# Performance work log

Hardware: AMD Instinct MI355X
Metric: run time of the kernel (lower is better)

Reference implementation:

```python
import jax, jax.numpy as jnp
import numpy as np

C, T, D = 32, 768, 100      # n_countries, n_times, n_ages (=n_features)
H = 5                        # attention heads (EncoderLayer default)
HID_GCN = 60                 # GCN hidden features
FFN = 64                     # feed_forward_dim
NPRED = 10                   # n_predictions
LHID = 200                   # hid_linear_part_dim
NL = 3                       # encoder layers


def setup_inputs() -> dict:
    key = jax.random.key(0)
    ks = jax.random.split(key, 24)
    s = 0.05
    rn = lambda k, shp: jax.random.normal(k, shp, jnp.float32) * s
    return {
        "X": jax.random.normal(ks[0], (C, T, D), jnp.float32),
        "A": jax.random.uniform(ks[1], (C, C), jnp.float32),
        # GCN params
        "gcn_w1": rn(ks[2], (D, HID_GCN)),
        "gcn_b1": rn(ks[3], (HID_GCN,)),
        "gcn_w2": rn(ks[4], (HID_GCN, D)),
        "gcn_b2": rn(ks[5], (D,)),
        # 3 stacked encoder layers
        "enc_wq": rn(ks[6], (NL, H, D, D)),
        "enc_wk": rn(ks[7], (NL, H, D, D)),
        "enc_wv": rn(ks[8], (NL, H, D, D)),
        "enc_wm": rn(ks[9], (NL, H * D, D)),
        "enc_f1w": rn(ks[10], (NL, D, FFN)),
        "enc_f1b": rn(ks[11], (NL, FFN)),
        "enc_f2w": rn(ks[12], (NL, FFN, D)),
        "enc_f2b": rn(ks[13], (NL, D)),
        "enc_ln1g": jnp.ones((NL, D), jnp.float32),
        "enc_ln1b": jnp.zeros((NL, D), jnp.float32),
        "enc_ln2g": jnp.ones((NL, D), jnp.float32),
        "enc_ln2b": jnp.zeros((NL, D), jnp.float32),
        "lin1_w": rn(ks[14], (D, LHID)),
        "lin1_b": rn(ks[15], (LHID,)),
        "lin2_w": rn(ks[16], (LHID, D)),
        "lin2_b": rn(ks[17], (D,)),
    }


def _layer_norm(x, g, b, eps=1e-5):
    m = x.mean(-1, keepdims=True)
    v = ((x - m) ** 2).mean(-1, keepdims=True)
    return (x - m) / jnp.sqrt(v + eps) * g + b


def _encoder_layer(x, wq, wk, wv, wm, f1w, f1b, f2w, f2b, g1, b1, g2, b2):
    # x: [C, T, D]; wq/wk/wv: [H, D, D]
    Q = jnp.einsum('ctd,hde->chte', x, wq)
    K = jnp.einsum('ctd,hde->chte', x, wk)
    V = jnp.einsum('ctd,hde->chte', x, wv)
    scores = jnp.einsum('chte,chse->chts', Q, K) / jnp.sqrt(jnp.float32(D))
    attn = jax.nn.softmax(scores, axis=-1)
    out = jnp.einsum('chts,chse->chte', attn, V)        # [C,H,T,D]
    out = out.transpose(0, 2, 1, 3).reshape(x.shape[0], x.shape[1], H * D)
    x = _layer_norm(x + out @ wm, g1, b1)
    ffn = jax.nn.relu(x @ f1w + f1b) @ f2w + f2b
    return _layer_norm(x + ffn, g2, b2)


def reference(X, A, gcn_w1, gcn_b1, gcn_w2, gcn_b2,
              enc_wq, enc_wk, enc_wv, enc_wm,
              enc_f1w, enc_f1b, enc_f2w, enc_f2b,
              enc_ln1g, enc_ln1b, enc_ln2g, enc_ln2b,
              lin1_w, lin1_b, lin2_w, lin2_b):
    n = A.shape[0]
    adj = A + jnp.eye(n, dtype=A.dtype)
    adj_hat = adj / adj.sum(-1, keepdims=True)
    # GCN layer 1
    h = jnp.einsum('ij,jta->ita', adj_hat, X)
    h = jnp.einsum('ita,ao->ito', h, gcn_w1) + gcn_b1
    h = jax.nn.relu(h)
    # GCN layer 2
    h = jnp.einsum('ij,jta->ita', adj_hat, h)
    h = jnp.einsum('ita,ao->ito', h, gcn_w2) + gcn_b2
    # 3 encoder layers (fixed structural loop)
    for l in range(NL):
        h = _encoder_layer(h, enc_wq[l], enc_wk[l], enc_wv[l], enc_wm[l],
                           enc_f1w[l], enc_f1b[l], enc_f2w[l], enc_f2b[l],
                           enc_ln1g[l], enc_ln1b[l], enc_ln2g[l], enc_ln2b[l])
    last = h[:, -1, :]  # [C, D]
    def step(carry, _):
        p = (carry @ lin1_w + lin1_b) @ lin2_w + lin2_b
        return p, p
    _, preds = jax.lax.scan(step, last, None, length=NPRED)  # [NPRED, C, D]
    return preds.transpose(1, 0, 2)  # [C, NPRED, D]
```

## Files before the change

kernel.cpp:

```cpp
#include <hip/hip_runtime.h>


#define ROWS 24576

#define OFF_ADJ   0L
#define OFF_X0    1024L
#define OFF_X1    (OFF_X0 + 2457600L)
#define OFF_XROW  (OFF_X1 + 3932160L)
#define OFF_XT    (OFF_XROW + 1572864L)
#define OFF_WBF   (OFF_XT + 1572864L)
#define OFF_MHT   (OFF_WBF + 6291456L)
#define OFF_USTT  (OFF_MHT + 122880L)
#define OFF_MP    (OFF_USTT + 98304L)
#define OFF_C0    (OFF_MP + 10000L)
#define OFF_F1WT  (OFF_C0 + 128L)
#define OFF_F2WT  (OFF_F1WT + 12288L)
#define OFF_GW1T  (OFF_F2WT + 10752L)
#define OFF_GW2T  (OFF_GW1T + 4096L)

typedef __attribute__((ext_vector_type(8))) short short8;
typedef __attribute__((ext_vector_type(4))) short short4v;
typedef __attribute__((ext_vector_type(4))) float float4v;
typedef __attribute__((ext_vector_type(2))) unsigned int uint2v;
typedef __attribute__((ext_vector_type(4))) unsigned int uint4v;

__device__ inline unsigned short f2bf(float f) {
    unsigned u = __builtin_bit_cast(unsigned, f);
    return (unsigned short)((u + 0x7fffu + ((u >> 16) & 1u)) >> 16);
}
__device__ inline unsigned pk2bf(float lo, float hi) {
    unsigned r;
    asm("v_cvt_pk_bf16_f32 %0, %1, %2" : "=v"(r) : "v"(lo), "v"(hi));
    return r;
}
__device__ inline void st4s(short* p, unsigned a, unsigned b) {
    *(short4v*)p = __builtin_bit_cast(short4v, (uint2v){a, b});
}
__device__ inline float bf2f(unsigned short v) {
    return __builtin_bit_cast(float, ((unsigned)v) << 16);
}
__device__ inline void gload16(const short* g, short* l) {
    __builtin_amdgcn_global_load_lds((const __attribute__((address_space(1))) void*)g,
                                     (__attribute__((address_space(3))) void*)l, 16, 0, 0);
}

__global__ void __launch_bounds__(256) k_mu2(const float* __restrict__ wq, const float* __restrict__ wk,
                                             const float* __restrict__ wv, const float* __restrict__ wm,
                                             const float* __restrict__ l1w, const float* __restrict__ l1b,
                                             const float* __restrict__ l2w, const float* __restrict__ l2b,
                                             const float* __restrict__ f1w, const float* __restrict__ f2w,
                                             const float* __restrict__ A,
                                             const float* __restrict__ gw1, const float* __restrict__ gw2,
                                             unsigned short* __restrict__ MhT, unsigned short* __restrict__ UstT,
                                             float* __restrict__ Mp, float* __restrict__ c0v,
                                             unsigned short* __restrict__ f1wT, unsigned short* __restrict__ f2wT,
                                             float* __restrict__ adjh,
                                             unsigned short* __restrict__ gw1T, unsigned short* __restrict__ gw2T) {
    int bi = blockIdx.x, tid = threadIdx.x;
    if (bi < 480) {
        int mat = bi >> 4, sub = bi & 15;
        int mode = mat / 15, idx = mat % 15, l = idx / 5, h = idx % 5;
        const float* Asrc = (mode == 0 ? wq : wv) + (l*5 + h)*10000;
        const float* Bsrc = (mode == 0) ? (wk + (l*5 + h)*10000) : (wm + l*50000 + h*10000);
        int oend = sub*625 + 625;
        for (int o = sub*625 + tid; o < oend; o += 256) {
            int r = o / 100, cix = o - (o/100)*100;
            const float* arow = Asrc + r*100;
            float acc = 0.f;
            if (mode == 0) {
                const float* brow = Bsrc + cix*100;
                for (int e = 0; e < 100; ++e) acc += arow[e] * brow[e];
                MhT[(long)(l*5 + h)*16384 + cix*128 + r] = f2bf(acc * 0.1f);
            } else {
                for (int e = 0; e < 100; ++e) acc += arow[e] * Bsrc[e*100 + cix];
                UstT[(long)l*65536 + (long)cix*512 + h*100 + r] = f2bf(acc);
            }
        }
        if (sub == 0) {
            if (mode == 0) {
                unsigned short* M0 = MhT + (long)(l*5 + h)*16384;
                for (int i = tid; i < 28*128; i += 256) M0[(100 + i/128)*128 + (i%128)] = 0;
                for (int i = tid; i < 100*28; i += 256) M0[(i/28)*128 + 100 + (i%28)] = 0;
            } else if (h == 4) {
                unsigned short* U0 = UstT + (long)l*65536;
                for (int i = tid; i < 28*512; i += 256) U0[(long)(100 + i/512)*512 + (i%512)] = 0;
                for (int i = tid; i < 100*12; i += 256) U0[(long)(i/12)*512 + 500 + (i%12)] = 0;
            }
        }
    } else if (bi < 496) {
        int sub = bi - 480;
        int oend = sub*625 + 625;
        for (int o = sub*625 + tid; o < oend; o += 256) {
            int r = o / 100, cix = o - (o/100)*100;
            const float* arow = l1w + r*200;
            float acc = 0.f;
            for (int e = 0; e < 200; ++e) acc += arow[e] * l2w[e*100 + cix];
            Mp[r*100 + cix] = acc;
        }
    } else if (bi == 496) {
        if (tid < 100) {
            float acc = l2b[tid];
            for (int e = 0; e < 200; ++e) acc += l1b[e] * l2w[e*100 + tid];
            c0v[tid] = acc;
        }
    } else if (bi < 500) {
        int l = bi - 497;
        unsigned short* F1 = f1wT + (long)l*8192;
        for (int i = tid; i < 8192; i += 256) {
            int o = i >> 7, k = i & 127;
            F1[i] = (k < 100) ? f2bf(f1w[l*6400 + k*64 + o]) : (unsigned short)0;
        }
        unsigned short* F2 = f2wT + (long)l*7168;
        for (int i = tid; i < 7168; i += 256) {
            int o2 = i >> 6, k2 = i & 63;
            F2[i] = (o2 < 100) ? f2bf(f2w[l*6400 + k2*100 + o2]) : (unsigned short)0;
        }
    } else if (bi == 500) {
        __shared__ float adj[1024];
        __shared__ float rs[32];
        for (int i = tid; i < 1024; i += 256) {
            int r = i >> 5, j = i & 31;
            adj[i] = A[i] + (r == j ? 1.f : 0.f);
        }
        __syncthreads();
        if (tid < 32) {
            float s = 0.f;
            #pragma unroll
            for (int jj = 0; jj < 32; ++jj) s += adj[tid*32 + jj];
            rs[tid] = s;
        }
        __syncthreads();
        for (int i = tid; i < 1024; i += 256) adjh[i] = adj[i] / rs[i >> 5];
    } else {
        for (int i = tid; i < 8192; i += 256) {
            int o = i >> 7, k = i & 127;
            gw1T[i] = (o < 60 && k < 100) ? f2bf(gw1[k*60 + o]) : (unsigned short)0;
        }
        for (int i = tid; i < 7168; i += 256) {
            int o = i >> 6, k = i & 63;
            gw2T[i] = (o < 100 && k < 60) ? f2bf(gw2[k*100 + o]) : (unsigned short)0;
        }
    }
}

__global__ void __launch_bounds__(128) k_gw1(const float* __restrict__ X,
                                             const unsigned short* __restrict__ gw1T,
                                             unsigned short* __restrict__ g) {
    const int tid = threadIdx.x, wave = tid >> 6, lane = tid & 63;
    const int l15 = lane & 15, l4 = lane >> 4;
    const long row = (long)blockIdx.x*32 + wave*16 + l15;
    const float* xrp = X + row*100;
    float4v acc[4];
    #pragma unroll
    for (int mt = 0; mt < 4; ++mt) acc[mt] = (float4v){0,0,0,0};
    #pragma unroll
    for (int ks = 0; ks < 4; ++ks) {
        short8 b;
        #pragma unroll
        for (int e = 0; e < 8; ++e) {
            int k = ks*32 + l4*8 + e;
            b[e] = (k < 100) ? (short)f2bf(xrp[k]) : (short)0;
        }
        #pragma unroll
        for (int mt = 0; mt < 4; ++mt) {
            short8 a = *(const short8*)((const short*)gw1T + (mt*16 + l15)*128 + ks*32 + l4*8);
            acc[mt] = __builtin_amdgcn_mfma_f32_16x16x32_bf16(a, b, acc[mt], 0, 0, 0);
        }
    }
    #pragma unroll
    for (int mt = 0; mt < 4; ++mt) {
        int o0 = mt*16 + l4*4;
        *(uint2v*)(g + row*64 + o0) =
            (uint2v){pk2bf(acc[mt][0], acc[mt][1]), pk2bf(acc[mt][2], acc[mt][3])};
    }
}

__global__ void __launch_bounds__(256) k_spmmg(const float* __restrict__ adjh,
                                               const unsigned short* __restrict__ g,
                                               const float* __restrict__ b1,
                                               unsigned short* __restrict__ hid) {
    __shared__ float adj[1024];
    int tid = threadIdx.x;
    for (int i = tid; i < 1024; i += 256) adj[i] = adjh[i];
    __syncthreads();
    long p = (long)blockIdx.x*256 + tid;
    int o = (int)(p & 63);
    float acc[32];
    #pragma unroll
    for (int i = 0; i < 32; ++i) acc[i] = 0.f;
    for (int j = 0; j < 32; ++j) {
        float xv = bf2f(g[(long)j*49152 + p]);
        #pragma unroll
        for (int i = 0; i < 32; ++i) acc[i] += adj[i*32 + j] * xv;
    }
    float bias = (o < 60) ? b1[o] : 0.f;
    #pragma unroll
    for (int i = 0; i < 32; ++i) hid[(long)i*49152 + p] = f2bf(fmaxf(acc[i] + bias, 0.f));
}

__global__ void __launch_bounds__(128) k_gw2(const unsigned short* __restrict__ hid,
                                             const unsigned short* __restrict__ gw2T,
                                             unsigned short* __restrict__ h2) {
    const int tid = threadIdx.x, wave = tid >> 6, lane = tid & 63;
    const int l15 = lane & 15, l4 = lane >> 4;
    const long row = (long)blockIdx.x*32 + wave*16 + l15;
    float4v acc[7];
    #pragma unroll
    for (int mt = 0; mt < 7; ++mt) acc[mt] = (float4v){0,0,0,0};
    #pragma unroll
    for (int ks = 0; ks < 2; ++ks) {
        short8 b = *(const short8*)((const short*)hid + row*64 + ks*32 + l4*8);
        #pragma unroll
        for (int mt = 0; mt < 7; ++mt) {
            short8 a = *(const short8*)((const short*)gw2T + (mt*16 + l15)*64 + ks*32 + l4*8);
            acc[mt] = __builtin_amdgcn_mfma_f32_16x16x32_bf16(a, b, acc[mt], 0, 0, 0);
        }
    }
    #pragma unroll
    for (int mt = 0; mt < 7; ++mt) {
        int o0 = mt*16 + l4*4;
        *(uint2v*)(h2 + row*128 + o0) =
            (uint2v){pk2bf(acc[mt][0], acc[mt][1]), pk2bf(acc[mt][2], acc[mt][3])};
    }
    *(uint2v*)(h2 + row*128 + 112 + l4*4) = (uint2v){0u, 0u};
}

__global__ void __launch_bounds__(384) k_spmmx(const float* __restrict__ adjh,
                                               const unsigned short* __restrict__ h2,
                                               const float* __restrict__ b2,
                                               float* __restrict__ x0,
                                               unsigned short* __restrict__ xrow,
                                               unsigned short* __restrict__ xT) {
    __shared__ float adj[1024];
    int tid = threadIdx.x;
    for (int i = tid; i < 1024; i += 384) adj[i] = adjh[i];
    __syncthreads();
    long p = (long)blockIdx.x*384 + tid;
    int o = (int)(p & 127);
    int t = (int)(p >> 7);
    float acc[32];
    #pragma unroll
    for (int i = 0; i < 32; ++i) acc[i] = 0.f;
    for (int j = 0; j < 32; ++j) {
        float xv = bf2f(h2[(long)j*98304 + p]);
        #pragma unroll
        for (int i = 0; i < 32; ++i) acc[i] += adj[i*32 + j] * xv;
    }
    if (o < 100) {
        float bias = b2[o];
        #pragma unroll
        for (int i = 0; i < 32; ++i) {
            float v = acc[i] + bias;
            x0[((long)i*768 + t)*100 + o] = v;
            unsigned short bv = f2bf(v);
            xrow[((long)i*768 + t)*128 + o] = bv;
            xT[(long)i*98304 + (long)o*768 + t] = bv;
        }
    } else {
        #pragma unroll
        for (int i = 0; i < 32; ++i) {
            xrow[((long)i*768 + t)*128 + o] = 0;
            if (o < 112) xT[(long)i*98304 + (long)o*768 + t] = 0;
        }
    }
}


__global__ void __launch_bounds__(256) k_attn12(const unsigned short* __restrict__ xrow,
                                                const unsigned short* __restrict__ xT,
                                                const unsigned short* __restrict__ MhT,
                                                unsigned short* __restrict__ Wb) {
    __shared__ __align__(16) short xr[2][64 * 128];
    __shared__ __align__(16) short xt[112 * 64];
    const int tid = threadIdx.x;
    const int wave = tid >> 6, lane = tid & 63;
    const int l15 = lane & 15, l4 = lane >> 4;
    const int c = blockIdx.z, h = blockIdx.y, q0 = blockIdx.x * 128;

    const short* xrg = (const short*)xrow + (long)c*768*128;
    const short* xtg = (const short*)xT + (long)c*128*768;
    const int rl4 = lane >> 4, cp16 = lane & 15;
    const int rl8 = lane >> 3, cp8 = lane & 7;
    const int njt = (wave == 3) ? 2 : 4;
    const int sw8 = (l15 & 7) << 3;
    const int swt = l15 & 7;

    #pragma unroll
    for (int j = 0; j < 4; ++j) {
        int row = wave*16 + j*4 + rl4;
        int lc = cp16 ^ (row & 7);
        gload16(xrg + (long)row*128 + lc*8, xr[0] + (wave*16 + j*4)*128);
    }

    short8 qb0[4], qb1[4];
    {
        short* mq = &xr[1][wave * 16 * 128];
        const short* Mb = (const short*)MhT + (long)h*16384 + l15*128 + l4*8;
        const short* xq = (const short*)xrow + ((long)c*768 + q0 + wave*16 + l15)*128 + l4*8;
        short8 bq0[4], bq1[4];
        #pragma unroll
        for (int kk = 0; kk < 4; ++kk) {
            bq0[kk] = *(const short8*)(xq + kk*32);
            bq1[kk] = *(const short8*)(xq + 64*128 + kk*32);
        }
        float4v qc0[8], qc1[8];
        #pragma unroll
        for (int mt = 0; mt < 8; ++mt) { qc0[mt] = (float4v){0,0,0,0}; qc1[mt] = (float4v){0,0,0,0}; }
        #pragma unroll
        for (int mt = 0; mt < 8; ++mt) {
            #pragma unroll
            for (int kk = 0; kk < 4; ++kk) {
                short8 a = *(const short8*)(Mb + (mt*16)*128 + kk*32);
                qc0[mt] = __builtin_amdgcn_mfma_f32_16x16x32_bf16(a, bq0[kk], qc0[mt], 0, 0, 0);
                qc1[mt] = __builtin_amdgcn_mfma_f32_16x16x32_bf16(a, bq1[kk], qc1[mt], 0, 0, 0);
            }
        }
        #pragma unroll
        for (int mt = 0; mt < 8; ++mt)
            st4s(mq + l15*128 + ((mt*16 + l4*4) ^ sw8),
                 pk2bf(qc0[mt][0], qc0[mt][1]), pk2bf(qc0[mt][2], qc0[mt][3]));
        asm volatile("" ::: "memory");
        #pragma unroll
        for (int kk = 0; kk < 4; ++kk)
            qb0[kk] = *(const short8*)(mq + l15*128 + ((kk*32 + l4*8) ^ sw8));
        asm volatile("" ::: "memory");
        #pragma unroll
        for (int mt = 0; mt < 8; ++mt)
            st4s(mq + l15*128 + ((mt*16 + l4*4) ^ sw8),
                 pk2bf(qc1[mt][0], qc1[mt][1]), pk2bf(qc1[mt][2], qc1[mt][3]));
        asm volatile("" ::: "memory");
        #pragma unroll
        for (int kk = 0; kk < 4; ++kk)
            qb1[kk] = *(const short8*)(mq + l15*128 + ((kk*32 + l4*8) ^ sw8));
    }

    __syncthreads();

    float4v o0[7], o1[7];
    #pragma unroll
    for (int n = 0; n < 7; ++n) { o0[n] = (float4v){0,0,0,0}; o1[n] = (float4v){0,0,0,0}; }
    float lsum0 = 0.f, lsum1 = 0.f;

    for (int kt = 0; kt < 12; ++kt) {
        const int key0 = kt * 64;
        const short* xrb = xr[kt & 1];

        for (int j = 0; j < njt; ++j) {
            int row = wave*32 + j*8 + rl8;
            int lc = cp8 ^ (row & 7);
            gload16(xtg + (long)row*768 + key0 + lc*8, xt + (wave*32 + j*8)*64);
        }
        if (kt < 11) {
            short* xrn = xr[(kt + 1) & 1];
            #pragma unroll
            for (int j = 0; j < 4; ++j) {
                int row = wave*16 + j*4 + rl4;
                int lc = cp16 ^ (row & 7);
                gload16(xrg + (long)(key0 + 64 + row)*128 + lc*8, xrn + (wave*16 + j*4)*128);
            }
        }
        __builtin_amdgcn_sched_barrier(0);

        unsigned pw0[4], pw1[4];
        #pragma unroll
        for (int kn = 0; kn < 2; ++kn) {
            float4v s0 = (float4v){0,0,0,0}, s1 = (float4v){0,0,0,0};
            #pragma unroll
            for (int kk = 0; kk < 4; ++kk) {
                short8 a = *(const short8*)(xrb + (kn*16 + l15)*128 + (((kk*4 + l4) ^ (l15 & 7))*8));
                s0 = __builtin_amdgcn_mfma_f32_16x16x32_bf16(a, qb0[kk], s0, 0, 0, 0);
                s1 = __builtin_amdgcn_mfma_f32_16x16x32_bf16(a, qb1[kk], s1, 0, 0, 0);
            }
            float p0[4], p1[4];
            #pragma unroll
            for (int r = 0; r < 4; ++r) {
                p0[r] = __expf(s0[r]); lsum0 += p0[r];
                p1[r] = __expf(s1[r]); lsum1 += p1[r];
            }
            pw0[kn*2]   = pk2bf(p0[0], p0[1]); pw0[kn*2+1] = pk2bf(p0[2], p0[3]);
            pw1[kn*2]   = pk2bf(p1[0], p1[1]); pw1[kn*2+1] = pk2bf(p1[2], p1[3]);
        }

        if (kt < 11) { asm volatile("s_waitcnt vmcnt(4)" ::: "memory"); }
        else         { asm volatile("s_waitcnt vmcnt(0)" ::: "memory"); }
        __builtin_amdgcn_s_barrier();

        {
            short8 b0 = __builtin_bit_cast(short8, (uint4v){pw0[0], pw0[1], pw0[2], pw0[3]});
            short8 b1 = __builtin_bit_cast(short8, (uint4v){pw1[0], pw1[1], pw1[2], pw1[3]});
            const int offLo = (((l4 >> 1) ^ swt) * 8) + (l4 & 1) * 4;
            const int offHi = (((2 + (l4 >> 1)) ^ swt) * 8) + (l4 & 1) * 4;
            #pragma unroll
            for (int dt = 0; dt < 7; ++dt) {
                const short* xrow_t = xt + (dt*16 + l15)*64;
                short4v lo = *(const short4v*)(xrow_t + offLo);
                short4v hi = *(const short4v*)(xrow_t + offHi);
                short8 a = __builtin_shufflevector(lo, hi, 0, 1, 2, 3, 4, 5, 6, 7);
                o0[dt] = __builtin_amdgcn_mfma_f32_16x16x32_bf16(a, b0, o0[dt], 0, 0, 0);
                o1[dt] = __builtin_amdgcn_mfma_f32_16x16x32_bf16(a, b1, o1[dt], 0, 0, 0);
            }
        }

        #pragma unroll
        for (int kn = 2; kn < 4; ++kn) {
            float4v s0 = (float4v){0,0,0,0}, s1 = (float4v){0,0,0,0};
            #pragma unroll
            for (int kk = 0; kk < 4; ++kk) {
                short8 a = *(const short8*)(xrb + (kn*16 + l15)*128 + (((kk*4 + l4) ^ (l15 & 7))*8));
                s0 = __builtin_amdgcn_mfma_f32_16x16x32_bf16(a, qb0[kk], s0, 0, 0, 0);
                s1 = __builtin_amdgcn_mfma_f32_16x16x32_bf16(a, qb1[kk], s1, 0, 0, 0);
            }
            float p0[4], p1[4];
            #pragma unroll
            for (int r = 0; r < 4; ++r) {
                p0[r] = __expf(s0[r]); lsum0 += p0[r];
                p1[r] = __expf(s1[r]); lsum1 += p1[r];
            }
            pw0[(kn-2)*2]   = pk2bf(p0[0], p0[1]); pw0[(kn-2)*2+1] = pk2bf(p0[2], p0[3]);
            pw1[(kn-2)*2]   = pk2bf(p1[0], p1[1]); pw1[(kn-2)*2+1] = pk2bf(p1[2], p1[3]);
        }

        {
            short8 b0 = __builtin_bit_cast(short8, (uint4v){pw0[0], pw0[1], pw0[2], pw0[3]});
            short8 b1 = __builtin_bit_cast(short8, (uint4v){pw1[0], pw1[1], pw1[2], pw1[3]});
            const int offLo = (((4 + (l4 >> 1)) ^ swt) * 8) + (l4 & 1) * 4;
            const int offHi = (((6 + (l4 >> 1)) ^ swt) * 8) + (l4 & 1) * 4;
            #pragma unroll
            for (int dt = 0; dt < 7; ++dt) {
                const short* xrow_t = xt + (dt*16 + l15)*64;
                short4v lo = *(const short4v*)(xrow_t + offLo);
                short4v hi = *(const short4v*)(xrow_t + offHi);
                short8 a = __builtin_shufflevector(lo, hi, 0, 1, 2, 3, 4, 5, 6, 7);
                o0[dt] = __builtin_amdgcn_mfma_f32_16x16x32_bf16(a, b0, o0[dt], 0, 0, 0);
                o1[dt] = __builtin_amdgcn_mfma_f32_16x16x32_bf16(a, b1, o1[dt], 0, 0, 0);
            }
        }
        __syncthreads();
    }

    float l0 = lsum0, l1 = lsum1;
    l0 += __shfl_xor(l0, 16, 64); l0 += __shfl_xor(l0, 32, 64);
    l1 += __shfl_xor(l1, 16, 64); l1 += __shfl_xor(l1, 32, 64);
    float inv0 = 1.f / l0, inv1 = 1.f / l1;

    unsigned short* Wo0 = Wb + ((long)(c*768 + q0 + wave*16 + l15))*512 + h*100 + l4*4;
    unsigned short* Wo1 = Wo0 + 64*512;
    #pragma unroll
    for (int dt = 0; dt < 7; ++dt) {
        if (dt < 6 || l4 == 0) {
            *(uint2v*)(Wo0 + dt*16) = (uint2v){pk2bf(o0[dt][0]*inv0, o0[dt][1]*inv0),
                                               pk2bf(o0[dt][2]*inv0, o0[dt][3]*inv0)};
            *(uint2v*)(Wo1 + dt*16) = (uint2v){pk2bf(o1[dt][0]*inv1, o1[dt][1]*inv1),
                                               pk2bf(o1[dt][2]*inv1, o1[dt][3]*inv1)};
        }
    }
    if (h == 0) {
        unsigned short* Wz = Wb + ((long)c*768 + q0)*512 + 500;
        for (int i = tid; i < 1536; i += 256) Wz[(long)(i/12)*512 + (i%12)] = 0;
    }
}

template<bool EMIT>
__global__ void __launch_bounds__(128) k_tail(const unsigned short* __restrict__ Wb,
        const unsigned short* __restrict__ UstT,
        const unsigned short* __restrict__ f1wT, const unsigned short* __restrict__ f2wT,
        const float* __restrict__ f1b, const float* __restrict__ f2b,
        const float* __restrict__ g1, const float* __restrict__ b1,
        const float* __restrict__ g2, const float* __restrict__ b2,
        float* __restrict__ x, unsigned short* __restrict__ xrow, unsigned short* __restrict__ xT) {
    __shared__ __align__(16) short zS[2][16*136];
    __shared__ __align__(16) short tS[2][16*72];
    const int tid = threadIdx.x, wave = tid >> 6, lane = tid & 63;
    const int l15 = lane & 15, l4 = lane >> 4;
    const long row = (long)blockIdx.x*32 + wave*16 + l15;
    const int cc = blockIdx.x / 24;
    const int tt = (blockIdx.x % 24)*32 + wave*16 + l15;
    short* myz = zS[wave];
    short* myt = tS[wave];

    const short* Wr = (const short*)Wb + row*512 + l4*8;
    float4v o[8];
    #pragma unroll
    for (int mt = 0; mt < 8; ++mt) o[mt] = (float4v){0,0,0,0};
    for (int ks = 0; ks < 16; ++ks) {
        short8 b = *(const short8*)(Wr + ks*32);
        #pragma unroll
        for (int mt = 0; mt < 8; ++mt) {
            short8 a = *(const short8*)((const short*)UstT + (long)(mt*16 + l15)*512 + ks*32 + l4*8);
            o[mt] = __builtin_amdgcn_mfma_f32_16x16x32_bf16(a, b, o[mt], 0, 0, 0);
        }
    }

    float zv[7][4];
    float sum = 0.f;
    #pragma unroll
    for (int mt = 0; mt < 7; ++mt) {
        int f0 = mt*16 + l4*4;
        float4 xv = {0,0,0,0};
        if (f0 < 100) xv = *(const float4*)(x + row*100 + f0);
        #pragma unroll
        for (int r = 0; r < 4; ++r) {
            float z = 0.f;
            if (f0 < 100) { z = o[mt][r] + ((const float*)&xv)[r]; sum += z; }
            zv[mt][r] = z;
        }
    }
    sum += __shfl_xor(sum, 16, 64); sum += __shfl_xor(sum, 32, 64);
    float mean = sum * 0.01f;
    float vs = 0.f;
    #pragma unroll
    for (int mt = 0; mt < 7; ++mt) {
        if (mt*16 + l4*4 < 100) {
            #pragma unroll
            for (int r = 0; r < 4; ++r) { float d = zv[mt][r] - mean; vs += d*d; }
        }
    }
    vs += __shfl_xor(vs, 16, 64); vs += __shfl_xor(vs, 32, 64);
    float inv = rsqrtf(vs * 0.01f + 1e-5f);
    float x1r[7][4];
    #pragma unroll
    for (int mt = 0; mt < 7; ++mt) {
        int f0 = mt*16 + l4*4;
        float4 gv = {0,0,0,0}, bv = {0,0,0,0};
        if (f0 < 100) { gv = *(const float4*)(g1 + f0); bv = *(const float4*)(b1 + f0); }
        #pragma unroll
        for (int r = 0; r < 4; ++r)
            x1r[mt][r] = (f0 < 100) ? (zv[mt][r] - mean) * inv * ((const float*)&gv)[r] + ((const float*)&bv)[r] : 0.f;
    }

    #pragma unroll
    for (int mt = 0; mt < 8; ++mt) {
        float v0 = (mt < 7) ? x1r[mt][0] : 0.f, v1 = (mt < 7) ? x1r[mt][1] : 0.f;
        float v2 = (mt < 7) ? x1r[mt][2] : 0.f, v3 = (mt < 7) ? x1r[mt][3] : 0.f;
        st4s(myz + l15*136 + mt*16 + l4*4, pk2bf(v0, v1), pk2bf(v2, v3));
    }
    asm volatile("" ::: "memory");

    float4v t2[4];
    #pragma unroll
    for (int m2t = 0; m2t < 4; ++m2t) t2[m2t] = (float4v){0,0,0,0};
    #pragma unroll
    for (int ks = 0; ks < 4; ++ks) {
        short8 b = *(const short8*)(myz + l15*136 + ks*32 + l4*8);
        #pragma unroll
        for (int m2t = 0; m2t < 4; ++m2t) {
            short8 a = *(const short8*)((const short*)f1wT + (m2t*16 + l15)*128 + ks*32 + l4*8);
            t2[m2t] = __builtin_amdgcn_mfma_f32_16x16x32_bf16(a, b, t2[m2t], 0, 0, 0);
        }
    }
    #pragma unroll
    for (int m2t = 0; m2t < 4; ++m2t) {
        int m20 = m2t*16 + l4*4;
        float4 bv = *(const float4*)(f1b + m20);
        float v0 = fmaxf(t2[m2t][0] + ((const float*)&bv)[0], 0.f);
        float v1 = fmaxf(t2[m2t][1] + ((const float*)&bv)[1], 0.f);
        float v2 = fmaxf(t2[m2t][2] + ((const float*)&bv)[2], 0.f);
        float v3 = fmaxf(t2[m2t][3] + ((const float*)&bv)[3], 0.f);
        st4s(myt + l15*72 + m20, pk2bf(v0, v1), pk2bf(v2, v3));
    }
    asm volatile("" ::: "memory");

    float4v o3[7];
    #pragma unroll
    for (int m3t = 0; m3t < 7; ++m3t) o3[m3t] = (float4v){0,0,0,0};
    #pragma unroll
    for (int ks2 = 0; ks2 < 2; ++ks2) {
        short8 b = *(const short8*)(myt + l15*72 + ks2*32 + l4*8);
        #pragma unroll
        for (int m3t = 0; m3t < 7; ++m3t) {
            short8 a = *(const short8*)((const short*)f2wT + (m3t*16 + l15)*64 + ks2*32 + l4*8);
            o3[m3t] = __builtin_amdgcn_mfma_f32_16x16x32_bf16(a, b, o3[m3t], 0, 0, 0);
        }
    }

    float z2[7][4];
    float sum2 = 0.f;
    #pragma unroll
    for (int m3t = 0; m3t < 7; ++m3t) {
        int f0 = m3t*16 + l4*4;
        float4 bv = {0,0,0,0};
        if (f0 < 100) bv = *(const float4*)(f2b + f0);
        #pragma unroll
        for (int r = 0; r < 4; ++r) {
            float z = 0.f;
            if (f0 < 100) { z = o3[m3t][r] + ((const float*)&bv)[r] + x1r[m3t][r]; sum2 += z; }
            z2[m3t][r] = z;
        }
    }
    sum2 += __shfl_xor(sum2, 16, 64); sum2 += __shfl_xor(sum2, 32, 64);
    float mean2 = sum2 * 0.01f;
    float vs2 = 0.f;
    #pragma unroll
    for (int m3t = 0; m3t < 7; ++m3t) {
        if (m3t*16 + l4*4 < 100) {
            #pragma unroll
            for (int r = 0; r < 4; ++r) { float d = z2[m3t][r] - mean2; vs2 += d*d; }
        }
    }
    vs2 += __shfl_xor(vs2, 16, 64); vs2 += __shfl_xor(vs2, 32, 64);
    float inv2 = rsqrtf(vs2 * 0.01f + 1e-5f);

    unsigned short* xTc = EMIT ? (xT + (long)cc*98304 + tt) : nullptr;
    #pragma unroll
    for (int m3t = 0; m3t < 7; ++m3t) {
        int f0 = m3t*16 + l4*4;
        if (f0 < 100) {
            float4 gv = *(const float4*)(g2 + f0);
            float4 bv = *(const float4*)(b2 + f0);
            float y[4];
            #pragma unroll
            for (int r = 0; r < 4; ++r)
                y[r] = (z2[m3t][r] - mean2) * inv2 * ((const float*)&gv)[r] + ((const float*)&bv)[r];
            *(float4*)(x + row*100 + f0) = (float4){y[0], y[1], y[2], y[3]};
            if (EMIT) {
                *(uint2v*)(xrow + row*128 + f0) = (uint2v){pk2bf(y[0], y[1]), pk2bf(y[2], y[3])};
                #pragma unroll
                for (int r = 0; r < 4; ++r)
                    xTc[(long)(f0 + r)*768] = f2bf(y[r]);
            }
        } else if (EMIT) {
            *(uint2v*)(xrow + row*128 + f0) = (uint2v){0u, 0u};
            #pragma unroll
            for (int r = 0; r < 4; ++r)
                if (f0 + r < 112) xTc[(long)(f0 + r)*768] = 0;
        }
    }
    if (EMIT) *(uint2v*)(xrow + row*128 + 112 + l4*4) = (uint2v){0u, 0u};
}

__global__ void __launch_bounds__(256) k_pred2(const float* __restrict__ xf,
        const float* __restrict__ Mp, const float* __restrict__ c0v,
        float* __restrict__ out) {
    int c = blockIdx.x, tid = threadIdx.x;
    __shared__ float Ml[10000];
    __shared__ float carry[100];
    for (int i = tid; i < 10000; i += 256) Ml[i] = Mp[i];
    if (tid < 100) carry[tid] = xf[((long)c*768 + 767)*100 + tid];
    __syncthreads();
    for (int s = 0; s < 10; ++s) {
        float pv = 0.f;
        if (tid < 100) {
            pv = c0v[tid];
            for (int d = 0; d < 100; ++d) pv += carry[d] * Ml[d*100 + tid];
            out[((long)c*10 + s)*100 + tid] = pv;
        }
        __syncthreads();
        if (tid < 100) carry[tid] = pv;
        __syncthreads();
    }
}

extern "C" void kernel_launch(void* const* d_in, const int* in_sizes, int n_in,
                              void* d_out, int out_size, void* d_ws, size_t ws_size,
                              hipStream_t stream) {
    const float* X    = (const float*)d_in[0];
    const float* A    = (const float*)d_in[1];
    const float* gw1  = (const float*)d_in[2];
    const float* gb1  = (const float*)d_in[3];
    const float* gw2  = (const float*)d_in[4];
    const float* gb2  = (const float*)d_in[5];
    const float* wq   = (const float*)d_in[6];
    const float* wk   = (const float*)d_in[7];
    const float* wv   = (const float*)d_in[8];
    const float* wm   = (const float*)d_in[9];
    const float* f1w  = (const float*)d_in[10];
    const float* f1b  = (const float*)d_in[11];
    const float* f2w  = (const float*)d_in[12];
    const float* f2b  = (const float*)d_in[13];
    const float* ln1g = (const float*)d_in[14];
    const float* ln1b = (const float*)d_in[15];
    const float* ln2g = (const float*)d_in[16];
    const float* ln2b = (const float*)d_in[17];
    const float* l1w  = (const float*)d_in[18];
    const float* l1b  = (const float*)d_in[19];
    const float* l2w  = (const float*)d_in[20];
    const float* l2b  = (const float*)d_in[21];
    (void)in_sizes; (void)n_in; (void)out_size; (void)ws_size;

    float* ws   = (float*)d_ws;
    float* adjh = ws + OFF_ADJ;
    float* x0   = ws + OFF_X0;
    unsigned short* gbuf = (unsigned short*)(ws + OFF_X1);
    unsigned short* hbuf = (unsigned short*)(ws + OFF_X1 + 786432L);
    unsigned short* h2buf= (unsigned short*)(ws + OFF_X1 + 1572864L);
    unsigned short* xrow = (unsigned short*)(ws + OFF_XROW);
    unsigned short* xTb  = (unsigned short*)(ws + OFF_XT);
    unsigned short* Wbf  = (unsigned short*)(ws + OFF_WBF);
    unsigned short* MhT  = (unsigned short*)(ws + OFF_MHT);
    unsigned short* UstT = (unsigned short*)(ws + OFF_USTT);
    float* Mp   = ws + OFF_MP;
    float* c0v  = ws + OFF_C0;
    unsigned short* f1wT = (unsigned short*)(ws + OFF_F1WT);
    unsigned short* f2wT = (unsigned short*)(ws + OFF_F2WT);
    unsigned short* gw1T = (unsigned short*)(ws + OFF_GW1T);
    unsigned short* gw2T = (unsigned short*)(ws + OFF_GW2T);
    float* out  = (float*)d_out;

    k_mu2<<<502, 256, 0, stream>>>(wq, wk, wv, wm, l1w, l1b, l2w, l2b, f1w, f2w, A, gw1, gw2,
                                   MhT, UstT, Mp, c0v, f1wT, f2wT, adjh, gw1T, gw2T);

    k_gw1<<<768, 128, 0, stream>>>(X, gw1T, gbuf);
    k_spmmg<<<192, 256, 0, stream>>>(adjh, gbuf, gb1, hbuf);
    k_gw2<<<768, 128, 0, stream>>>(hbuf, gw2T, h2buf);
    k_spmmx<<<256, 384, 0, stream>>>(adjh, h2buf, gb2, x0, xrow, xTb);

    for (int l = 0; l < 3; ++l) {
        k_attn12<<<dim3(6,5,32), 256, 0, stream>>>(xrow, xTb, MhT + (long)l*81920, Wbf);
        if (l < 2)
            k_tail<true><<<768, 128, 0, stream>>>(Wbf, UstT + (long)l*65536,
                f1wT + (long)l*8192, f2wT + (long)l*7168, f1b + l*64, f2b + l*100,
                ln1g + l*100, ln1b + l*100, ln2g + l*100, ln2b + l*100, x0, xrow, xTb);
        else
            k_tail<false><<<768, 128, 0, stream>>>(Wbf, UstT + (long)l*65536,
                f1wT + (long)l*8192, f2wT + (long)l*7168, f1b + l*64, f2b + l*100,
                ln1g + l*100, ln1b + l*100, ln2g + l*100, ln2b + l*100, x0, xrow, xTb);
    }

    k_pred2<<<32, 256, 0, stream>>>(x0, Mp, c0v, out);
}
```

Measured before the change: 508.6 us.

## Stage UstT tiles through double-buffered LDS in k_tail with prefetched W rows

k_tail used to read the shared UstT weight matrix straight from global memory inside the MFMA loop. It now copies 64-column chunks into a swizzled, double-buffered LDS tile with async global-to-LDS loads, prefetching the next chunk and the next W fragments while the current chunk feeds the MFMAs. The LDS scratch for the later z/t stages is carved out of the same buffers to keep shared memory use flat. In k_attn12, the second-half P fragments now go into separate registers instead of reusing pw0/pw1, which may help scheduling but raises register pressure.

```diff
diff --git a/kernel.cpp b/kernel.cpp
--- a/kernel.cpp
+++ b/kernel.cpp
@@ -265,7 +265,6 @@
     }
 }
 
-
 __global__ void __launch_bounds__(256) k_attn12(const unsigned short* __restrict__ xrow,
                                                 const unsigned short* __restrict__ xT,
                                                 const unsigned short* __restrict__ MhT,
@@ -401,6 +400,7 @@
             }
         }
 
+        unsigned pw0b[4], pw1b[4];
         #pragma unroll
         for (int kn = 2; kn < 4; ++kn) {
             float4v s0 = (float4v){0,0,0,0}, s1 = (float4v){0,0,0,0};
@@ -416,13 +416,13 @@
                 p0[r] = __expf(s0[r]); lsum0 += p0[r];
                 p1[r] = __expf(s1[r]); lsum1 += p1[r];
             }
-            pw0[(kn-2)*2]   = pk2bf(p0[0], p0[1]); pw0[(kn-2)*2+1] = pk2bf(p0[2], p0[3]);
-            pw1[(kn-2)*2]   = pk2bf(p1[0], p1[1]); pw1[(kn-2)*2+1] = pk2bf(p1[2], p1[3]);
+            pw0b[(kn-2)*2]   = pk2bf(p0[0], p0[1]); pw0b[(kn-2)*2+1] = pk2bf(p0[2], p0[3]);
+            pw1b[(kn-2)*2]   = pk2bf(p1[0], p1[1]); pw1b[(kn-2)*2+1] = pk2bf(p1[2], p1[3]);
         }
 
         {
-            short8 b0 = __builtin_bit_cast(short8, (uint4v){pw0[0], pw0[1], pw0[2], pw0[3]});
-            short8 b1 = __builtin_bit_cast(short8, (uint4v){pw1[0], pw1[1], pw1[2], pw1[3]});
+            short8 b0 = __builtin_bit_cast(short8, (uint4v){pw0b[0], pw0b[1], pw0b[2], pw0b[3]});
+            short8 b1 = __builtin_bit_cast(short8, (uint4v){pw1b[0], pw1b[1], pw1b[2], pw1b[3]});
             const int offLo = (((4 + (l4 >> 1)) ^ swt) * 8) + (l4 & 1) * 4;
             const int offHi = (((6 + (l4 >> 1)) ^ swt) * 8) + (l4 & 1) * 4;
             #pragma unroll
@@ -468,28 +468,64 @@
         const float* __restrict__ g1, const float* __restrict__ b1,
         const float* __restrict__ g2, const float* __restrict__ b2,
         float* __restrict__ x, unsigned short* __restrict__ xrow, unsigned short* __restrict__ xT) {
-    __shared__ __align__(16) short zS[2][16*136];
-    __shared__ __align__(16) short tS[2][16*72];
+    __shared__ __align__(16) short ust[2][128 * 64];
     const int tid = threadIdx.x, wave = tid >> 6, lane = tid & 63;
     const int l15 = lane & 15, l4 = lane >> 4;
     const long row = (long)blockIdx.x*32 + wave*16 + l15;
     const int cc = blockIdx.x / 24;
     const int tt = (blockIdx.x % 24)*32 + wave*16 + l15;
-    short* myz = zS[wave];
-    short* myt = tS[wave];
+    const int sr8 = lane >> 3, sc8 = lane & 7;
 
     const short* Wr = (const short*)Wb + row*512 + l4*8;
     float4v o[8];
     #pragma unroll
     for (int mt = 0; mt < 8; ++mt) o[mt] = (float4v){0,0,0,0};
-    for (int ks = 0; ks < 16; ++ks) {
-        short8 b = *(const short8*)(Wr + ks*32);
+
+    {
+        short* dst = ust[0];
+        #pragma unroll
+        for (int j = 0; j < 8; ++j) {
+            int r = wave*64 + j*8 + sr8;
+            int lc = sc8 ^ (r & 7);
+            gload16((const short*)UstT + (long)r*512 + 0 + lc*8, dst + (wave*64 + j*8)*64);
+        }
+    }
+    __syncthreads();
+
+    short8 bc0 = *(const short8*)(Wr + 0);
+    short8 bc1 = *(const short8*)(Wr + 32);
+    for (int cb = 0; cb < 8; ++cb) {
+        if (cb < 7) {
+            const int ksb = (cb + 1) * 64;
+            short* dst = ust[(cb + 1) & 1];
+            #pragma unroll
+            for (int j = 0; j < 8; ++j) {
+                int r = wave*64 + j*8 + sr8;
+                int lc = sc8 ^ (r & 7);
+                gload16((const short*)UstT + (long)r*512 + ksb + lc*8, dst + (wave*64 + j*8)*64);
+            }
+        }
+        short8 bn0, bn1;
+        if (cb < 7) {
+            bn0 = *(const short8*)(Wr + (cb*2 + 2)*32);
+            bn1 = *(const short8*)(Wr + (cb*2 + 3)*32);
+        }
+        __builtin_amdgcn_sched_barrier(0);
+
+        const short* bufc = ust[cb & 1];
         #pragma unroll
         for (int mt = 0; mt < 8; ++mt) {
-            short8 a = *(const short8*)((const short*)UstT + (long)(mt*16 + l15)*512 + ks*32 + l4*8);
-            o[mt] = __builtin_amdgcn_mfma_f32_16x16x32_bf16(a, b, o[mt], 0, 0, 0);
-        }
-    }
+            short8 a0 = *(const short8*)(bufc + (mt*16 + l15)*64 + (((0*4 + l4) ^ (l15 & 7))*8));
+            o[mt] = __builtin_amdgcn_mfma_f32_16x16x32_bf16(a0, bc0, o[mt], 0, 0, 0);
+            short8 a1 = *(const short8*)(bufc + (mt*16 + l15)*64 + (((1*4 + l4) ^ (l15 & 7))*8));
+            o[mt] = __builtin_amdgcn_mfma_f32_16x16x32_bf16(a1, bc1, o[mt], 0, 0, 0);
+        }
+        bc0 = bn0; bc1 = bn1;
+        __syncthreads();
+    }
+
+    short* myz = ust[0] + wave * 2176;
+    short* myt = ust[1] + wave * 1152;
 
     float zv[7][4];
     float sum = 0.f;
```

After: 466.6 us. 8.3% less time.
